# Optimization experiments

Measured on AMD Instinct MI355X. Metric: run time of the kernel, lower is better.

## Reference

```python
import jax, jax.numpy as jnp
import numpy as np

N = 10000
E = 160000
UNITS = 64
NUM_RBF = 32
CUTOFF = 1.0


def _xavier(k, shape):
    fan_out, fan_in = shape
    lim = float(np.sqrt(6.0 / (fan_in + fan_out)))
    return jax.random.uniform(k, shape, minval=-lim, maxval=lim, dtype=jnp.float32)


def setup_inputs() -> dict:
    key = jax.random.key(0)
    ks = jax.random.split(key, 16)
    inp = {
        "edge_index": jax.random.randint(ks[0], (2, E), 0, N),
        "edge_weight": jax.random.uniform(ks[1], (E,), dtype=jnp.float32),
        "edge_attr": jax.random.normal(ks[2], (E, NUM_RBF), dtype=jnp.float32),
        "X": jax.random.normal(ks[3], (N, UNITS, 3, 3), dtype=jnp.float32),
        # scalar MLP: num_rbf -> units -> 2*units -> 3*units
        "Ws0": _xavier(ks[4], (UNITS, NUM_RBF)), "bs0": jnp.zeros((UNITS,), jnp.float32),
        "Ws1": _xavier(ks[5], (2 * UNITS, UNITS)), "bs1": jnp.zeros((2 * UNITS,), jnp.float32),
        "Ws2": _xavier(ks[6], (3 * UNITS, 2 * UNITS)), "bs2": jnp.zeros((3 * UNITS,), jnp.float32),
    }
    for i in range(6):
        inp[f"Wt{i}"] = _xavier(ks[7 + i], (UNITS, UNITS))
    return inp


def cosine_cutoff(r, cutoff):
    return jnp.where(r < cutoff, 0.5 * (jnp.cos(jnp.pi * r / cutoff) + 1.0), 0.0)


def tensor_norm(X):
    # X: [N, units, 3, 3] -> [N, units]
    return jnp.sum(X * X, axis=(-2, -1))


def decompose_tensor(X):
    eye = jnp.eye(3, dtype=X.dtype)
    trace = jnp.trace(X, axis1=-2, axis2=-1)  # [N, units]
    I = (trace / 3.0)[..., None, None] * eye
    A = 0.5 * (X - jnp.swapaxes(X, -2, -1))
    S = 0.5 * (X + jnp.swapaxes(X, -2, -1)) - I
    return I, A, S


def channel_linear(T, W):
    # linear over the channel dim: [N, c, 3, 3] x [d, c] -> [N, d, 3, 3]
    return jnp.einsum('ncij,dc->ndij', T, W)


def reference(edge_index, edge_weight, edge_attr, X,
              Ws0, bs0, Ws1, bs1, Ws2, bs2,
              Wt0, Wt1, Wt2, Wt3, Wt4, Wt5):
    act = jax.nn.silu
    C = cosine_cutoff(edge_weight, CUTOFF)  # [E]
    h = act(edge_attr @ Ws0.T + bs0)
    h = act(h @ Ws1.T + bs1)
    h = act(h @ Ws2.T + bs2)  # [E, 3*units]
    ea = (h * C[:, None]).reshape(h.shape[0], UNITS, 3)  # [E, units, 3]

    X = X / (tensor_norm(X) + 1.0)[..., None, None]
    I, A, S = decompose_tensor(X)
    I = channel_linear(I, Wt0)
    A = channel_linear(A, Wt1)
    S = channel_linear(S, Wt2)
    Y = I + A + S

    src, dst = edge_index[0], edge_index[1]
    n = X.shape[0]
    # message = per-edge radial scaling of gathered node tensors; aggregate at src
    Im = jax.ops.segment_sum(ea[..., 0, None, None] * I[dst], src, num_segments=n)
    Am = jax.ops.segment_sum(ea[..., 1, None, None] * A[dst], src, num_segments=n)
    Sm = jax.ops.segment_sum(ea[..., 2, None, None] * S[dst], src, num_segments=n)
    msg = Im + Am + Sm

    # O(3): symmetrized product of batched 3x3 matmuls
    AB = jnp.matmul(msg, Y) + jnp.matmul(Y, msg)
    I2, A2, S2 = decompose_tensor(AB)
    normp1 = (tensor_norm(I2 + A2 + S2) + 1.0)[..., None, None]
    I2 = channel_linear(I2 / normp1, Wt3)
    A2 = channel_linear(A2 / normp1, Wt4)
    S2 = channel_linear(S2 / normp1, Wt5)
    dX = I2 + A2 + S2
    return X + dX + jnp.matmul(dX, dX)
```

## Files before the change

kernel.cpp:

```cpp
#include <hip/hip_runtime.h>
#include <math.h>

#define NN 10000
#define EE 160000

#define OFF_WTT 0
#define OFF_PK  24576
#define OFF_B2P 41984
#define OFF_IASH 42176
#define OFF_EAH 3242176
#define OFF_INT 18602176

typedef __attribute__((ext_vector_type(8))) _Float16 h16x8;
typedef __attribute__((ext_vector_type(2))) __fp16 fp16x2_raw;
typedef __attribute__((ext_vector_type(4))) float f32x4;

__device__ __forceinline__ float silu_f(float x) {
    return x * __builtin_amdgcn_rcpf(1.0f + __expf(-x));
}
__device__ __forceinline__ unsigned int pkh(float a, float b) {
    union { fp16x2_raw h; unsigned int u; } cv;
    cv.h = __builtin_amdgcn_cvt_pkrtz(a, b);
    return cv.u;
}
__device__ __forceinline__ unsigned short f2h(float f) {
    union { _Float16 h; unsigned short u; } cv; cv.h = (_Float16)f; return cv.u;
}
__device__ __forceinline__ float h2f(unsigned short s) {
    union { unsigned short u; _Float16 h; } cv; cv.u = s; return (float)cv.h;
}
__device__ __forceinline__ float h2f_lo(unsigned int u) { return h2f((unsigned short)(u & 0xffffu)); }
__device__ __forceinline__ float h2f_hi(unsigned int u) { return h2f((unsigned short)(u >> 16)); }

__global__ void k_prep(const float* __restrict__ Wt0, const float* __restrict__ Wt1,
                       const float* __restrict__ Wt2, const float* __restrict__ Wt3,
                       const float* __restrict__ Wt4, const float* __restrict__ Wt5,
                       const float* __restrict__ Ws0, const float* __restrict__ Ws1,
                       const float* __restrict__ Ws2, const float* __restrict__ bs2,
                       const int* __restrict__ ei,
                       float* __restrict__ WtT, unsigned short* __restrict__ PK,
                       float* __restrict__ bs2p, int* __restrict__ counts) {
    int idx = blockIdx.x * 256 + threadIdx.x;
    if (idx < 24576) {
        int k = idx >> 12, r = idx & 4095;
        int c = r >> 6, d = r & 63;
        const float* W = (k == 0) ? Wt0 : (k == 1) ? Wt1 : (k == 2) ? Wt2
                       : (k == 3) ? Wt3 : (k == 4) ? Wt4 : Wt5;
        WtT[idx] = W[d * 64 + c];
    } else if (idx < 26624) {
        int q = idx - 24576;
        int ot = q >> 9, r = q & 511, lane = r >> 3, j = r & 7;
        int k = ((lane >> 4) * 8) + j, o = ot * 16 + (lane & 15);
        PK[q] = f2h(Ws0[o * 32 + k]);
    } else if (idx < 34816) {
        int q = idx - 24576;
        int i = q - 2048, ch = i >> 9, r = i & 511, lane = r >> 3, j = r & 7;
        int ot = ch >> 1, ks = ch & 1;
        int k = ks * 32 + (lane >> 4) * 8 + j, o = ot * 16 + (lane & 15);
        PK[q] = f2h(Ws1[o * 64 + k]);
    } else if (idx < 59392) {
        int q = idx - 24576;
        int i = q - 10240, ch = i >> 9, r = i & 511, lane = r >> 3, j = r & 7;
        int ot = ch >> 2, ks = ch & 3;
        int k = ks * 32 + (lane >> 4) * 8 + j;
        int op = ot * 16 + (lane & 15);
        int o = (op & 63) * 3 + (op >> 6);
        PK[q] = f2h(Ws2[o * 128 + k]);
    } else if (idx < 59584) {
        int op = idx - 59392;
        bs2p[op] = bs2[(op & 63) * 3 + (op >> 6)];
    } else if (idx < 59584 + EE) {
        int e = idx - 59584;
        atomicAdd(&counts[ei[e]], 1);
    }
}

__global__ __launch_bounds__(256) void k_scan(const int* __restrict__ counts,
                                              int* __restrict__ offsets) {
    __shared__ int sums[256];
    int t = threadIdx.x;
    int base = t * 40;
    int s = 0;
    if (base < NN) {
        const int4* p = (const int4*)(counts + base);
#pragma unroll
        for (int q = 0; q < 10; ++q) { int4 a = p[q]; s += a.x + a.y + a.z + a.w; }
    }
    sums[t] = s;
    __syncthreads();
    for (int off = 1; off < 256; off <<= 1) {
        int tmp = (t >= off) ? sums[t - off] : 0;
        __syncthreads();
        sums[t] += tmp;
        __syncthreads();
    }
    int run = sums[t] - s;
    if (base < NN) {
        const int4* p = (const int4*)(counts + base);
#pragma unroll
        for (int q = 0; q < 10; ++q) {
            int4 a = p[q];
            offsets[base + 4 * q + 0] = run; run += a.x;
            offsets[base + 4 * q + 1] = run; run += a.y;
            offsets[base + 4 * q + 2] = run; run += a.z;
            offsets[base + 4 * q + 3] = run; run += a.w;
        }
    }
    if (t == 255) offsets[NN] = run;
}

__global__ void k_fill(const int* __restrict__ ei, const int* __restrict__ offsets,
                       int* __restrict__ cursor, int* __restrict__ bucket,
                       int* __restrict__ dstp) {
    int e = blockIdx.x * 256 + threadIdx.x;
    if (e < EE) {
        int s = ei[e];
        int pos = offsets[s] + atomicAdd(&cursor[s], 1);
        bucket[pos] = e;
        dstp[pos] = ei[EE + e];
    }
}

__global__ __launch_bounds__(256) void k_nodeprep(const float* __restrict__ X,
                                                  const float* __restrict__ WtT,
                                                  unsigned int* __restrict__ IASu) {
    int t = threadIdx.x, w = t >> 6, c = t & 63;
    int n = blockIdx.x * 4 + w;
    __shared__ float XS[4][576];
    __shared__ float L[4][64][12];
    float* xs = XS[w];
#pragma unroll
    for (int i = 0; i < 9; i++) xs[c + 64 * i] = X[(size_t)n * 576 + c + 64 * i];
    __builtin_amdgcn_wave_barrier();
    float x[9];
#pragma unroll
    for (int j = 0; j < 9; j++) x[j] = xs[c * 9 + j];
    float nrm = 0.f;
#pragma unroll
    for (int j = 0; j < 9; j++) nrm += x[j] * x[j];
    float inv = __builtin_amdgcn_rcpf(nrm + 1.0f);
#pragma unroll
    for (int j = 0; j < 9; j++) x[j] *= inv;
    float tr3 = (x[0] + x[4] + x[8]) * (1.0f / 3.0f);
    L[w][c][0] = tr3;
    L[w][c][1] = 0.5f * (x[1] - x[3]);
    L[w][c][2] = 0.5f * (x[2] - x[6]);
    L[w][c][3] = 0.5f * (x[5] - x[7]);
    L[w][c][4] = x[0] - tr3;
    L[w][c][5] = x[4] - tr3;
    L[w][c][6] = 0.5f * (x[1] + x[3]);
    L[w][c][7] = 0.5f * (x[2] + x[6]);
    L[w][c][8] = 0.5f * (x[5] + x[7]);
    __builtin_amdgcn_wave_barrier();
    int d = c;
    const float* W0 = WtT;
    const float* W1 = WtT + 4096;
    const float* W2 = WtT + 8192;
    float aI = 0, aA0 = 0, aA1 = 0, aA2 = 0, aS0 = 0, aS1 = 0, aS2 = 0, aS3 = 0, aS4 = 0;
    for (int cc = 0; cc < 64; ++cc) {
        float w0 = W0[cc * 64 + d], w1 = W1[cc * 64 + d], w2 = W2[cc * 64 + d];
        float4 L0 = *(const float4*)&L[w][cc][0];
        float4 L1 = *(const float4*)&L[w][cc][4];
        float L8 = L[w][cc][8];
        aI  += w0 * L0.x;
        aA0 += w1 * L0.y; aA1 += w1 * L0.z; aA2 += w1 * L0.w;
        aS0 += w2 * L1.x; aS1 += w2 * L1.y; aS2 += w2 * L1.z;
        aS3 += w2 * L1.w; aS4 += w2 * L8;
    }
    unsigned int* op = IASu + (size_t)n * 320 + d;
    op[0]   = pkh(aI, aA0);
    op[64]  = pkh(aA1, aA2);
    op[128] = pkh(aS0, aS1);
    op[192] = pkh(aS2, aS3);
    op[256] = pkh(aS4, 0.0f);
}

__global__ __launch_bounds__(256) void k_mlp(const float* __restrict__ attr,
                                             const float* __restrict__ ew,
                                             const int* __restrict__ bucket,
                                             const unsigned short* __restrict__ PK,
                                             const float* __restrict__ bs0,
                                             const float* __restrict__ bs1,
                                             const float* __restrict__ bs2p,
                                             unsigned short* __restrict__ eah) {
    __shared__ unsigned short H[4][16][152];
    int t = threadIdx.x;
    int l = t & 63, w = t >> 6, lr = l & 15, lg = l >> 4;
    int pos = blockIdx.x * 64 + w * 16 + lr;
    int eid = bucket[pos];
    const float* ap = attr + (size_t)eid * 32 + lg * 8;
    float4 av0 = *(const float4*)ap;
    float4 av1 = *(const float4*)(ap + 4);
    union { h16x8 h; unsigned int u[4]; } B1;
    B1.u[0] = pkh(av0.x, av0.y); B1.u[1] = pkh(av0.z, av0.w);
    B1.u[2] = pkh(av1.x, av1.y); B1.u[3] = pkh(av1.z, av1.w);
    float rw = ew[eid];
    float C = (rw < 1.0f) ? 0.5f * (cosf(3.14159265358979f * rw) + 1.0f) : 0.0f;

    const h16x8* P1 = (const h16x8*)PK;
    const h16x8* P2 = (const h16x8*)(PK + 2048);
    const h16x8* P3 = (const h16x8*)(PK + 10240);

#pragma unroll
    for (int ot = 0; ot < 4; ++ot) {
        float4 bb = *(const float4*)&bs0[ot * 16 + lg * 4];
        f32x4 acc = {bb.x, bb.y, bb.z, bb.w};
        acc = __builtin_amdgcn_mfma_f32_16x16x32_f16(P1[ot * 64 + l], B1.h, acc, 0, 0, 0);
        unsigned int u01 = pkh(silu_f(acc[0]), silu_f(acc[1]));
        unsigned int u23 = pkh(silu_f(acc[2]), silu_f(acc[3]));
        *(uint2*)&H[w][lr][ot * 16 + lg * 4] = make_uint2(u01, u23);
    }
    __builtin_amdgcn_wave_barrier();

    h16x8 B2a = *(const h16x8*)&H[w][lr][lg * 8];
    h16x8 B2b = *(const h16x8*)&H[w][lr][32 + lg * 8];
    __builtin_amdgcn_wave_barrier();
#pragma unroll
    for (int ot = 0; ot < 8; ++ot) {
        float4 bb = *(const float4*)&bs1[ot * 16 + lg * 4];
        f32x4 acc = {bb.x, bb.y, bb.z, bb.w};
        acc = __builtin_amdgcn_mfma_f32_16x16x32_f16(P2[(ot * 2 + 0) * 64 + l], B2a, acc, 0, 0, 0);
        acc = __builtin_amdgcn_mfma_f32_16x16x32_f16(P2[(ot * 2 + 1) * 64 + l], B2b, acc, 0, 0, 0);
        unsigned int u01 = pkh(silu_f(acc[0]), silu_f(acc[1]));
        unsigned int u23 = pkh(silu_f(acc[2]), silu_f(acc[3]));
        *(uint2*)&H[w][lr][ot * 16 + lg * 4] = make_uint2(u01, u23);
    }
    __builtin_amdgcn_wave_barrier();

    h16x8 B3[4];
#pragma unroll
    for (int ks = 0; ks < 4; ++ks)
        B3[ks] = *(const h16x8*)&H[w][lr][ks * 32 + lg * 8];
    size_t ebase = (size_t)pos * 192;
#pragma unroll
    for (int ot = 0; ot < 12; ++ot) {
        float4 bb = *(const float4*)&bs2p[ot * 16 + lg * 4];
        f32x4 acc = {bb.x, bb.y, bb.z, bb.w};
#pragma unroll
        for (int ks = 0; ks < 4; ++ks)
            acc = __builtin_amdgcn_mfma_f32_16x16x32_f16(P3[(ot * 4 + ks) * 64 + l], B3[ks], acc, 0, 0, 0);
        unsigned int u01 = pkh(silu_f(acc[0]) * C, silu_f(acc[1]) * C);
        unsigned int u23 = pkh(silu_f(acc[2]) * C, silu_f(acc[3]) * C);
        *(uint2*)&eah[ebase + ot * 16 + lg * 4] = make_uint2(u01, u23);
    }
}

__global__ __launch_bounds__(256) void k_aggout(const int* __restrict__ offsets,
                                                const int* __restrict__ dstp,
                                                const unsigned short* __restrict__ eah,
                                                const unsigned int* __restrict__ IASu,
                                                const float* __restrict__ X,
                                                const float* __restrict__ WtT,
                                                float* __restrict__ out) {
    int t = threadIdx.x, w = t >> 6, c = t & 63;
    int n = blockIdx.x * 4 + w;
    __shared__ float XS[4][576];
    __shared__ float LO[4][768];
    float* xs = XS[w];
    float* lo = LO[w];
#pragma unroll
    for (int i = 0; i < 9; i++) xs[c + 64 * i] = X[(size_t)n * 576 + c + 64 * i];

    int beg = offsets[n], end = offsets[n + 1];
    float m0 = 0, m1 = 0, m2 = 0, m3 = 0, m4 = 0, m5 = 0, m6 = 0, m7 = 0, m8 = 0;
    int i = beg;
    for (; i + 2 <= end; i += 2) {
        int d0 = dstp[i], d1 = dstp[i + 1];
        const unsigned short* ep0 = eah + (size_t)i * 192;
        const unsigned short* ep1 = ep0 + 192;
        float a00 = h2f(ep0[c]), a01 = h2f(ep0[64 + c]), a02 = h2f(ep0[128 + c]);
        float a10 = h2f(ep1[c]), a11 = h2f(ep1[64 + c]), a12 = h2f(ep1[128 + c]);
        const unsigned int* p0 = IASu + (size_t)d0 * 320 + c;
        const unsigned int* p1 = IASu + (size_t)d1 * 320 + c;
        unsigned int u00 = p0[0], u01 = p0[64], u02 = p0[128], u03 = p0[192], u04 = p0[256];
        unsigned int u10 = p1[0], u11 = p1[64], u12 = p1[128], u13 = p1[192], u14 = p1[256];
        m0 += a00 * h2f_lo(u00) + a10 * h2f_lo(u10);
        m1 += a01 * h2f_hi(u00) + a11 * h2f_hi(u10);
        m2 += a01 * h2f_lo(u01) + a11 * h2f_lo(u11);
        m3 += a01 * h2f_hi(u01) + a11 * h2f_hi(u11);
        m4 += a02 * h2f_lo(u02) + a12 * h2f_lo(u12);
        m5 += a02 * h2f_hi(u02) + a12 * h2f_hi(u12);
        m6 += a02 * h2f_lo(u03) + a12 * h2f_lo(u13);
        m7 += a02 * h2f_hi(u03) + a12 * h2f_hi(u13);
        m8 += a02 * h2f_lo(u04) + a12 * h2f_lo(u14);
    }
    if (i < end) {
        int d0 = dstp[i];
        const unsigned short* ep0 = eah + (size_t)i * 192;
        float a00 = h2f(ep0[c]), a01 = h2f(ep0[64 + c]), a02 = h2f(ep0[128 + c]);
        const unsigned int* p0 = IASu + (size_t)d0 * 320 + c;
        unsigned int u00 = p0[0], u01 = p0[64], u02 = p0[128], u03 = p0[192], u04 = p0[256];
        m0 += a00 * h2f_lo(u00); m1 += a01 * h2f_hi(u00);
        m2 += a01 * h2f_lo(u01); m3 += a01 * h2f_hi(u01);
        m4 += a02 * h2f_lo(u02); m5 += a02 * h2f_hi(u02);
        m6 += a02 * h2f_lo(u03); m7 += a02 * h2f_hi(u03);
        m8 += a02 * h2f_lo(u04);
    }
    const unsigned int* yp = IASu + (size_t)n * 320 + c;
    unsigned int y0 = yp[0], y1 = yp[64], y2 = yp[128], y3 = yp[192], y4 = yp[256];
    float yI = h2f_lo(y0), yA0 = h2f_hi(y0), yA1 = h2f_lo(y1), yA2 = h2f_hi(y1);
    float yS0 = h2f_lo(y2), yS1 = h2f_hi(y2), yS2 = h2f_lo(y3), yS3 = h2f_hi(y3);
    float yS4 = h2f_lo(y4);

    float M[3][3] = {
        { m0 + m4,   m1 + m6,  m2 + m7 },
        { -m1 + m6,  m0 + m5,  m3 + m8 },
        { -m2 + m7, -m3 + m8,  m0 - m4 - m5 } };
    float Y[3][3] = {
        { yI + yS0,   yA0 + yS2,  yA1 + yS3 },
        { -yA0 + yS2, yI + yS1,   yA2 + yS4 },
        { -yA1 + yS3, -yA2 + yS4, yI - yS0 - yS1 } };
    float AB[3][3];
#pragma unroll
    for (int ii = 0; ii < 3; ii++)
#pragma unroll
        for (int j = 0; j < 3; j++) {
            float s = 0.f;
#pragma unroll
            for (int k = 0; k < 3; k++) s += M[ii][k] * Y[k][j] + Y[ii][k] * M[k][j];
            AB[ii][j] = s;
        }
    float tr3 = (AB[0][0] + AB[1][1] + AB[2][2]) * (1.0f / 3.0f);
    float fro = 0.f;
#pragma unroll
    for (int ii = 0; ii < 3; ii++)
#pragma unroll
        for (int j = 0; j < 3; j++) fro += AB[ii][j] * AB[ii][j];
    float inv = __builtin_amdgcn_rcpf(fro + 1.0f);
    float (*L12)[12] = (float (*)[12])lo;
    L12[c][0] = tr3 * inv;
    L12[c][1] = 0.5f * (AB[0][1] - AB[1][0]) * inv;
    L12[c][2] = 0.5f * (AB[0][2] - AB[2][0]) * inv;
    L12[c][3] = 0.5f * (AB[1][2] - AB[2][1]) * inv;
    L12[c][4] = (AB[0][0] - tr3) * inv;
    L12[c][5] = (AB[1][1] - tr3) * inv;
    L12[c][6] = 0.5f * (AB[0][1] + AB[1][0]) * inv;
    L12[c][7] = 0.5f * (AB[0][2] + AB[2][0]) * inv;
    L12[c][8] = 0.5f * (AB[1][2] + AB[2][1]) * inv;
    __builtin_amdgcn_wave_barrier();
    int d = c;
    const float* W3 = WtT + 3 * 4096;
    const float* W4 = WtT + 4 * 4096;
    const float* W5 = WtT + 5 * 4096;
    float aI = 0, aA0 = 0, aA1 = 0, aA2 = 0, aS0 = 0, aS1 = 0, aS2 = 0, aS3 = 0, aS4 = 0;
    for (int cc = 0; cc < 64; ++cc) {
        float w3 = W3[cc * 64 + d], w4 = W4[cc * 64 + d], w5 = W5[cc * 64 + d];
        float4 L0 = *(const float4*)&L12[cc][0];
        float4 L1 = *(const float4*)&L12[cc][4];
        float L8 = L12[cc][8];
        aI  += w3 * L0.x;
        aA0 += w4 * L0.y; aA1 += w4 * L0.z; aA2 += w4 * L0.w;
        aS0 += w5 * L1.x; aS1 += w5 * L1.y; aS2 += w5 * L1.z;
        aS3 += w5 * L1.w; aS4 += w5 * L8;
    }
    float dX[3][3] = {
        { aI + aS0,   aA0 + aS2,  aA1 + aS3 },
        { -aA0 + aS2, aI + aS1,   aA2 + aS4 },
        { -aA1 + aS3, -aA2 + aS4, aI - aS0 - aS1 } };
    float D2[3][3];
#pragma unroll
    for (int ii = 0; ii < 3; ii++)
#pragma unroll
        for (int j = 0; j < 3; j++) {
            float s = 0.f;
#pragma unroll
            for (int k = 0; k < 3; k++) s += dX[ii][k] * dX[k][j];
            D2[ii][j] = s;
        }
    float x[9];
    __builtin_amdgcn_wave_barrier();
#pragma unroll
    for (int j = 0; j < 9; j++) x[j] = xs[d * 9 + j];
    float nrm = 0.f;
#pragma unroll
    for (int j = 0; j < 9; j++) nrm += x[j] * x[j];
    float xinv = __builtin_amdgcn_rcpf(nrm + 1.0f);
    __builtin_amdgcn_wave_barrier();
#pragma unroll
    for (int ii = 0; ii < 3; ii++)
#pragma unroll
        for (int j = 0; j < 3; j++)
            lo[d * 9 + ii * 3 + j] = x[ii * 3 + j] * xinv + dX[ii][j] + D2[ii][j];
    __builtin_amdgcn_wave_barrier();
#pragma unroll
    for (int ii = 0; ii < 9; ii++) out[(size_t)n * 576 + c + 64 * ii] = lo[c + 64 * ii];
}

extern "C" void kernel_launch(void* const* d_in, const int* in_sizes, int n_in,
                              void* d_out, int out_size, void* d_ws, size_t ws_size,
                              hipStream_t stream) {
    (void)in_sizes; (void)n_in; (void)out_size; (void)ws_size;
    const int* ei = (const int*)d_in[0];
    const float* ew = (const float*)d_in[1];
    const float* attr = (const float*)d_in[2];
    const float* X = (const float*)d_in[3];
    const float* Ws0 = (const float*)d_in[4];
    const float* bs0 = (const float*)d_in[5];
    const float* Ws1 = (const float*)d_in[6];
    const float* bs1 = (const float*)d_in[7];
    const float* Ws2 = (const float*)d_in[8];
    const float* bs2 = (const float*)d_in[9];
    const float* Wt0 = (const float*)d_in[10];
    const float* Wt1 = (const float*)d_in[11];
    const float* Wt2 = (const float*)d_in[12];
    const float* Wt3 = (const float*)d_in[13];
    const float* Wt4 = (const float*)d_in[14];
    const float* Wt5 = (const float*)d_in[15];
    float* ws = (float*)d_ws;
    int* ibase = (int*)(ws + OFF_INT);
    int* counts = ibase;
    int* cursor = ibase + NN;
    int* offsets = ibase + 2 * NN;
    int* bucket = ibase + 3 * NN + 1;
    int* dstp = bucket + EE;
    unsigned short* PK = (unsigned short*)(ws + OFF_PK);
    unsigned int* IASu = (unsigned int*)(ws + OFF_IASH);
    unsigned short* eah = (unsigned short*)(ws + OFF_EAH);

    (void)hipMemsetAsync(counts, 0, 2 * NN * sizeof(int), stream);
    k_prep<<<(59584 + EE + 255) / 256, 256, 0, stream>>>(
        Wt0, Wt1, Wt2, Wt3, Wt4, Wt5, Ws0, Ws1, Ws2, bs2, ei,
        ws, PK, ws + OFF_B2P, counts);
    k_scan<<<1, 256, 0, stream>>>(counts, offsets);
    k_fill<<<(EE + 255) / 256, 256, 0, stream>>>(ei, offsets, cursor, bucket, dstp);
    k_nodeprep<<<NN / 4, 256, 0, stream>>>(X, ws, IASu);
    k_mlp<<<EE / 64, 256, 0, stream>>>(attr, ew, bucket, PK, bs0, bs1, ws + OFF_B2P, eah);
    k_aggout<<<NN / 4, 256, 0, stream>>>(offsets, dstp, eah, IASu, X, ws, (float*)d_out);
}
```

Before: 162.8 us.

## Fuse edge MLP into per-node aggregation kernel, drop edge-attribute buffer

The separate edge-MLP kernel is merged into the aggregation/output kernel. Each wave now runs the three-layer MLP on its node's incoming edges in tiles of 16, writes the scaled radial features to shared memory and consumes them right away, so the global fp16 edge buffer and its write and read-back go away. In exchange, nodes with few edges leave MFMA rows idle in partially filled tiles, per-node edge-count imbalance adds wave divergence, and the larger shared-memory footprint may lower occupancy.

Result: slower. 276.4 us (+69.7%).

```diff
diff --git a/kernel.cpp b/kernel.cpp
--- a/kernel.cpp
+++ b/kernel.cpp
@@ -8,8 +8,7 @@
 #define OFF_PK  24576
 #define OFF_B2P 41984
 #define OFF_IASH 42176
-#define OFF_EAH 3242176
-#define OFF_INT 18602176
+#define OFF_INT 3242176
 
 typedef __attribute__((ext_vector_type(8))) _Float16 h16x8;
 typedef __attribute__((ext_vector_type(2))) __fp16 fp16x2_raw;
@@ -175,127 +174,117 @@
     op[256] = pkh(aS4, 0.0f);
 }
 
-__global__ __launch_bounds__(256) void k_mlp(const float* __restrict__ attr,
-                                             const float* __restrict__ ew,
-                                             const int* __restrict__ bucket,
-                                             const unsigned short* __restrict__ PK,
-                                             const float* __restrict__ bs0,
-                                             const float* __restrict__ bs1,
-                                             const float* __restrict__ bs2p,
-                                             unsigned short* __restrict__ eah) {
-    __shared__ unsigned short H[4][16][152];
-    int t = threadIdx.x;
-    int l = t & 63, w = t >> 6, lr = l & 15, lg = l >> 4;
-    int pos = blockIdx.x * 64 + w * 16 + lr;
-    int eid = bucket[pos];
-    const float* ap = attr + (size_t)eid * 32 + lg * 8;
-    float4 av0 = *(const float4*)ap;
-    float4 av1 = *(const float4*)(ap + 4);
-    union { h16x8 h; unsigned int u[4]; } B1;
-    B1.u[0] = pkh(av0.x, av0.y); B1.u[1] = pkh(av0.z, av0.w);
-    B1.u[2] = pkh(av1.x, av1.y); B1.u[3] = pkh(av1.z, av1.w);
-    float rw = ew[eid];
-    float C = (rw < 1.0f) ? 0.5f * (cosf(3.14159265358979f * rw) + 1.0f) : 0.0f;
-
+__global__ __launch_bounds__(256) void k_fused(const int* __restrict__ offsets,
+                                               const int* __restrict__ bucket,
+                                               const int* __restrict__ dstp,
+                                               const float* __restrict__ attr,
+                                               const float* __restrict__ ew,
+                                               const unsigned short* __restrict__ PK,
+                                               const float* __restrict__ bs0,
+                                               const float* __restrict__ bs1,
+                                               const float* __restrict__ bs2p,
+                                               const unsigned int* __restrict__ IASu,
+                                               const float* __restrict__ X,
+                                               const float* __restrict__ WtT,
+                                               float* __restrict__ out) {
+    __shared__ unsigned short SH[4][5312];
+    int t = threadIdx.x, w = t >> 6, l = t & 63;
+    int lr = l & 15, lg = l >> 4;
+    int n = blockIdx.x * 4 + w;
+    unsigned short* Hh = SH[w];
+    unsigned short* EAh = SH[w] + 2176;
+    int beg = offsets[n], end = offsets[n + 1];
     const h16x8* P1 = (const h16x8*)PK;
     const h16x8* P2 = (const h16x8*)(PK + 2048);
     const h16x8* P3 = (const h16x8*)(PK + 10240);
-
-#pragma unroll
-    for (int ot = 0; ot < 4; ++ot) {
-        float4 bb = *(const float4*)&bs0[ot * 16 + lg * 4];
-        f32x4 acc = {bb.x, bb.y, bb.z, bb.w};
-        acc = __builtin_amdgcn_mfma_f32_16x16x32_f16(P1[ot * 64 + l], B1.h, acc, 0, 0, 0);
-        unsigned int u01 = pkh(silu_f(acc[0]), silu_f(acc[1]));
-        unsigned int u23 = pkh(silu_f(acc[2]), silu_f(acc[3]));
-        *(uint2*)&H[w][lr][ot * 16 + lg * 4] = make_uint2(u01, u23);
-    }
-    __builtin_amdgcn_wave_barrier();
-
-    h16x8 B2a = *(const h16x8*)&H[w][lr][lg * 8];
-    h16x8 B2b = *(const h16x8*)&H[w][lr][32 + lg * 8];
-    __builtin_amdgcn_wave_barrier();
-#pragma unroll
-    for (int ot = 0; ot < 8; ++ot) {
-        float4 bb = *(const float4*)&bs1[ot * 16 + lg * 4];
-        f32x4 acc = {bb.x, bb.y, bb.z, bb.w};
-        acc = __builtin_amdgcn_mfma_f32_16x16x32_f16(P2[(ot * 2 + 0) * 64 + l], B2a, acc, 0, 0, 0);
-        acc = __builtin_amdgcn_mfma_f32_16x16x32_f16(P2[(ot * 2 + 1) * 64 + l], B2b, acc, 0, 0, 0);
-        unsigned int u01 = pkh(silu_f(acc[0]), silu_f(acc[1]));
-        unsigned int u23 = pkh(silu_f(acc[2]), silu_f(acc[3]));
-        *(uint2*)&H[w][lr][ot * 16 + lg * 4] = make_uint2(u01, u23);
-    }
-    __builtin_amdgcn_wave_barrier();
-
-    h16x8 B3[4];
-#pragma unroll
-    for (int ks = 0; ks < 4; ++ks)
-        B3[ks] = *(const h16x8*)&H[w][lr][ks * 32 + lg * 8];
-    size_t ebase = (size_t)pos * 192;
-#pragma unroll
-    for (int ot = 0; ot < 12; ++ot) {
-        float4 bb = *(const float4*)&bs2p[ot * 16 + lg * 4];
-        f32x4 acc = {bb.x, bb.y, bb.z, bb.w};
+    float m0 = 0, m1 = 0, m2 = 0, m3 = 0, m4 = 0, m5 = 0, m6 = 0, m7 = 0, m8 = 0;
+
+    for (int tb = beg; tb < end; tb += 16) {
+        int p = tb + lr;
+        bool valid = p < end;
+        int eid = bucket[valid ? p : beg];
+        const float* ap = attr + (size_t)eid * 32 + lg * 8;
+        float4 a0 = *(const float4*)ap;
+        float4 a1 = *(const float4*)(ap + 4);
+        union { h16x8 h; unsigned int u[4]; } B1;
+        B1.u[0] = pkh(a0.x, a0.y); B1.u[1] = pkh(a0.z, a0.w);
+        B1.u[2] = pkh(a1.x, a1.y); B1.u[3] = pkh(a1.z, a1.w);
+        float rw = ew[eid];
+        float C = (valid && rw < 1.0f) ? 0.5f * (cosf(3.14159265358979f * rw) + 1.0f) : 0.0f;
+
+#pragma unroll
+        for (int ot = 0; ot < 4; ++ot) {
+            h16x8 wf = P1[ot * 64 + l];
+            float4 bb = *(const float4*)&bs0[ot * 16 + lg * 4];
+            f32x4 acc = {bb.x, bb.y, bb.z, bb.w};
+            acc = __builtin_amdgcn_mfma_f32_16x16x32_f16(wf, B1.h, acc, 0, 0, 0);
+            unsigned int u01 = pkh(silu_f(acc[0]), silu_f(acc[1]));
+            unsigned int u23 = pkh(silu_f(acc[2]), silu_f(acc[3]));
+            *(uint2*)&Hh[lr * 136 + ot * 16 + lg * 4] = make_uint2(u01, u23);
+        }
+        __builtin_amdgcn_wave_barrier();
+        h16x8 B2a = *(const h16x8*)&Hh[lr * 136 + lg * 8];
+        h16x8 B2b = *(const h16x8*)&Hh[lr * 136 + 32 + lg * 8];
+        __builtin_amdgcn_wave_barrier();
+#pragma unroll
+        for (int ot = 0; ot < 8; ++ot) {
+            h16x8 wf0 = P2[(ot * 2 + 0) * 64 + l];
+            h16x8 wf1 = P2[(ot * 2 + 1) * 64 + l];
+            float4 bb = *(const float4*)&bs1[ot * 16 + lg * 4];
+            f32x4 acc = {bb.x, bb.y, bb.z, bb.w};
+            acc = __builtin_amdgcn_mfma_f32_16x16x32_f16(wf0, B2a, acc, 0, 0, 0);
+            acc = __builtin_amdgcn_mfma_f32_16x16x32_f16(wf1, B2b, acc, 0, 0, 0);
+            unsigned int u01 = pkh(silu_f(acc[0]), silu_f(acc[1]));
+            unsigned int u23 = pkh(silu_f(acc[2]), silu_f(acc[3]));
+            *(uint2*)&Hh[lr * 136 + ot * 16 + lg * 4] = make_uint2(u01, u23);
+        }
+        __builtin_amdgcn_wave_barrier();
+        h16x8 B3[4];
 #pragma unroll
         for (int ks = 0; ks < 4; ++ks)
-            acc = __builtin_amdgcn_mfma_f32_16x16x32_f16(P3[(ot * 4 + ks) * 64 + l], B3[ks], acc, 0, 0, 0);
-        unsigned int u01 = pkh(silu_f(acc[0]) * C, silu_f(acc[1]) * C);
-        unsigned int u23 = pkh(silu_f(acc[2]) * C, silu_f(acc[3]) * C);
-        *(uint2*)&eah[ebase + ot * 16 + lg * 4] = make_uint2(u01, u23);
-    }
-}
-
-__global__ __launch_bounds__(256) void k_aggout(const int* __restrict__ offsets,
-                                                const int* __restrict__ dstp,
-                                                const unsigned short* __restrict__ eah,
-                                                const unsigned int* __restrict__ IASu,
-                                                const float* __restrict__ X,
-                                                const float* __restrict__ WtT,
-                                                float* __restrict__ out) {
-    int t = threadIdx.x, w = t >> 6, c = t & 63;
-    int n = blockIdx.x * 4 + w;
-    __shared__ float XS[4][576];
-    __shared__ float LO[4][768];
-    float* xs = XS[w];
-    float* lo = LO[w];
+            B3[ks] = *(const h16x8*)&Hh[lr * 136 + ks * 32 + lg * 8];
+        __builtin_amdgcn_wave_barrier();
+#pragma unroll
+        for (int ot = 0; ot < 12; ++ot) {
+            h16x8 wf0 = P3[(ot * 4 + 0) * 64 + l];
+            h16x8 wf1 = P3[(ot * 4 + 1) * 64 + l];
+            h16x8 wf2 = P3[(ot * 4 + 2) * 64 + l];
+            h16x8 wf3 = P3[(ot * 4 + 3) * 64 + l];
+            float4 bb = *(const float4*)&bs2p[ot * 16 + lg * 4];
+            f32x4 acc = {bb.x, bb.y, bb.z, bb.w};
+            acc = __builtin_amdgcn_mfma_f32_16x16x32_f16(wf0, B3[0], acc, 0, 0, 0);
+            acc = __builtin_amdgcn_mfma_f32_16x16x32_f16(wf1, B3[1], acc, 0, 0, 0);
+            acc = __builtin_amdgcn_mfma_f32_16x16x32_f16(wf2, B3[2], acc, 0, 0, 0);
+            acc = __builtin_amdgcn_mfma_f32_16x16x32_f16(wf3, B3[3], acc, 0, 0, 0);
+            unsigned int u01 = pkh(silu_f(acc[0]) * C, silu_f(acc[1]) * C);
+            unsigned int u23 = pkh(silu_f(acc[2]) * C, silu_f(acc[3]) * C);
+            *(uint2*)&EAh[lr * 196 + ot * 16 + lg * 4] = make_uint2(u01, u23);
+        }
+        __builtin_amdgcn_wave_barrier();
+        int dstv = valid ? dstp[p] : 0;
+        int cnt = (end - tb < 16) ? (end - tb) : 16;
+        for (int te = 0; te < cnt; ++te) {
+            float ea0 = h2f(EAh[te * 196 + l]);
+            float ea1 = h2f(EAh[te * 196 + 64 + l]);
+            float ea2 = h2f(EAh[te * 196 + 128 + l]);
+            int dst = __shfl(dstv, te);
+            const unsigned int* pp = IASu + (size_t)dst * 320 + l;
+            unsigned int u0 = pp[0], u1 = pp[64], u2 = pp[128], u3 = pp[192], u4 = pp[256];
+            m0 += ea0 * h2f_lo(u0); m1 += ea1 * h2f_hi(u0);
+            m2 += ea1 * h2f_lo(u1); m3 += ea1 * h2f_hi(u1);
+            m4 += ea2 * h2f_lo(u2); m5 += ea2 * h2f_hi(u2);
+            m6 += ea2 * h2f_lo(u3); m7 += ea2 * h2f_hi(u3);
+            m8 += ea2 * h2f_lo(u4);
+        }
+        __builtin_amdgcn_wave_barrier();
+    }
+
+    int c = l;
+    float* xs = (float*)SH[w];
+    float* lo = xs + 576;
+    __builtin_amdgcn_wave_barrier();
 #pragma unroll
     for (int i = 0; i < 9; i++) xs[c + 64 * i] = X[(size_t)n * 576 + c + 64 * i];
-
-    int beg = offsets[n], end = offsets[n + 1];
-    float m0 = 0, m1 = 0, m2 = 0, m3 = 0, m4 = 0, m5 = 0, m6 = 0, m7 = 0, m8 = 0;
-    int i = beg;
-    for (; i + 2 <= end; i += 2) {
-        int d0 = dstp[i], d1 = dstp[i + 1];
-        const unsigned short* ep0 = eah + (size_t)i * 192;
-        const unsigned short* ep1 = ep0 + 192;
-        float a00 = h2f(ep0[c]), a01 = h2f(ep0[64 + c]), a02 = h2f(ep0[128 + c]);
-        float a10 = h2f(ep1[c]), a11 = h2f(ep1[64 + c]), a12 = h2f(ep1[128 + c]);
-        const unsigned int* p0 = IASu + (size_t)d0 * 320 + c;
-        const unsigned int* p1 = IASu + (size_t)d1 * 320 + c;
-        unsigned int u00 = p0[0], u01 = p0[64], u02 = p0[128], u03 = p0[192], u04 = p0[256];
-        unsigned int u10 = p1[0], u11 = p1[64], u12 = p1[128], u13 = p1[192], u14 = p1[256];
-        m0 += a00 * h2f_lo(u00) + a10 * h2f_lo(u10);
-        m1 += a01 * h2f_hi(u00) + a11 * h2f_hi(u10);
-        m2 += a01 * h2f_lo(u01) + a11 * h2f_lo(u11);
-        m3 += a01 * h2f_hi(u01) + a11 * h2f_hi(u11);
-        m4 += a02 * h2f_lo(u02) + a12 * h2f_lo(u12);
-        m5 += a02 * h2f_hi(u02) + a12 * h2f_hi(u12);
-        m6 += a02 * h2f_lo(u03) + a12 * h2f_lo(u13);
-        m7 += a02 * h2f_hi(u03) + a12 * h2f_hi(u13);
-        m8 += a02 * h2f_lo(u04) + a12 * h2f_lo(u14);
-    }
-    if (i < end) {
-        int d0 = dstp[i];
-        const unsigned short* ep0 = eah + (size_t)i * 192;
-        float a00 = h2f(ep0[c]), a01 = h2f(ep0[64 + c]), a02 = h2f(ep0[128 + c]);
-        const unsigned int* p0 = IASu + (size_t)d0 * 320 + c;
-        unsigned int u00 = p0[0], u01 = p0[64], u02 = p0[128], u03 = p0[192], u04 = p0[256];
-        m0 += a00 * h2f_lo(u00); m1 += a01 * h2f_hi(u00);
-        m2 += a01 * h2f_lo(u01); m3 += a01 * h2f_hi(u01);
-        m4 += a02 * h2f_lo(u02); m5 += a02 * h2f_hi(u02);
-        m6 += a02 * h2f_lo(u03); m7 += a02 * h2f_hi(u03);
-        m8 += a02 * h2f_lo(u04);
-    }
     const unsigned int* yp = IASu + (size_t)n * 320 + c;
     unsigned int y0 = yp[0], y1 = yp[64], y2 = yp[128], y3 = yp[192], y4 = yp[256];
     float yI = h2f_lo(y0), yA0 = h2f_hi(y0), yA1 = h2f_lo(y1), yA2 = h2f_hi(y1);
@@ -415,7 +404,6 @@
     int* dstp = bucket + EE;
     unsigned short* PK = (unsigned short*)(ws + OFF_PK);
     unsigned int* IASu = (unsigned int*)(ws + OFF_IASH);
-    unsigned short* eah = (unsigned short*)(ws + OFF_EAH);
 
     (void)hipMemsetAsync(counts, 0, 2 * NN * sizeof(int), stream);
     k_prep<<<(59584 + EE + 255) / 256, 256, 0, stream>>>(
@@ -424,6 +412,6 @@
     k_scan<<<1, 256, 0, stream>>>(counts, offsets);
     k_fill<<<(EE + 255) / 256, 256, 0, stream>>>(ei, offsets, cursor, bucket, dstp);
     k_nodeprep<<<NN / 4, 256, 0, stream>>>(X, ws, IASu);
-    k_mlp<<<EE / 64, 256, 0, stream>>>(attr, ew, bucket, PK, bs0, bs1, ws + OFF_B2P, eah);
-    k_aggout<<<NN / 4, 256, 0, stream>>>(offsets, dstp, eah, IASu, X, ws, (float*)d_out);
-}
+    k_fused<<<NN / 4, 256, 0, stream>>>(offsets, bucket, dstp, attr, ew, PK,
+                                        bs0, bs1, ws + OFF_B2P, IASu, X, ws, (float*)d_out);
+}
```
